# Kernel tuning notes

Hardware: AMD Instinct MI355X
Metric: run time of the kernel (lower is better)

Reference implementation:

```python
import jax, jax.numpy as jnp
import numpy as np

N = 100_000   # nodes
E = 3_200_000 # edges
F = 13        # input features
H = 64        # hidden dim
G = 512       # graphs in batch
C = 2         # output classes
BN_EPS = 1e-5


def _linear(key, fan_in, fan_out):
    kw, kb = jax.random.split(key)
    bound = 1.0 / np.sqrt(fan_in)
    W = jax.random.uniform(kw, (fan_in, fan_out), jnp.float32, -bound, bound)
    b = jax.random.uniform(kb, (fan_out,), jnp.float32, -bound, bound)
    return W, b


def _conv_params(key, fin, fout):
    k1, k2, k3 = jax.random.split(key, 3)
    W1, b1 = _linear(k1, fin, fout)
    W2, b2 = _linear(k2, fout, fout)
    gamma = jnp.ones((fout,), jnp.float32)
    beta = jnp.zeros((fout,), jnp.float32)
    mean = jax.random.normal(k3, (fout,), jnp.float32) * 0.1
    var = jnp.ones((fout,), jnp.float32)
    return W1, b1, gamma, beta, mean, var, W2, b2


def setup_inputs() -> dict:
    key = jax.random.key(0)
    ks = jax.random.split(key, 10)
    x = jax.random.normal(ks[0], (N, F), jnp.float32)
    src = jax.random.randint(ks[1], (E,), 0, N, jnp.int32)
    dst = jax.random.randint(ks[2], (E,), 0, N, jnp.int32)
    batch = jnp.sort(jax.random.randint(ks[3], (N,), 0, G, jnp.int32))
    inp = {"x": x, "src": src, "dst": dst, "batch": batch}
    for i, name in enumerate(["c1", "c2", "c3"]):
        fin = F if i == 0 else H
        W1, b1, g, be, m, v, W2, b2 = _conv_params(ks[4 + i], fin, H)
        inp.update({f"{name}_W1": W1, f"{name}_b1": b1, f"{name}_g": g,
                    f"{name}_be": be, f"{name}_m": m, f"{name}_v": v,
                    f"{name}_W2": W2, f"{name}_b2": b2})
    inp["fc1_W"], inp["fc1_b"] = _linear(ks[7], 3 * H, 3 * H)
    inp["fc2_W"], inp["fc2_b"] = _linear(ks[8], 3 * H, C)
    return inp


def _mlp(h, W1, b1, g, be, m, v, W2, b2):
    # Linear -> BatchNorm1d (inference, running stats) -> ReLU -> Linear -> ReLU
    h = h @ W1 + b1
    h = (h - m) * jax.lax.rsqrt(v + BN_EPS) * g + be
    h = jax.nn.relu(h)
    return jax.nn.relu(h @ W2 + b2)


def _gin_conv(x, src, dst, mlp_params):
    # GINConv with eps=0: MLP(x + sum_{j->i} x_j) via scatter-add over edges
    agg = jax.ops.segment_sum(x[src], dst, num_segments=N)
    return _mlp(x + agg, *mlp_params)


def reference(x, src, dst, batch,
              c1_W1, c1_b1, c1_g, c1_be, c1_m, c1_v, c1_W2, c1_b2,
              c2_W1, c2_b1, c2_g, c2_be, c2_m, c2_v, c2_W2, c2_b2,
              c3_W1, c3_b1, c3_g, c3_be, c3_m, c3_v, c3_W2, c3_b2,
              fc1_W, fc1_b, fc2_W, fc2_b):
    h1 = jax.nn.relu(_gin_conv(x, src, dst, (c1_W1, c1_b1, c1_g, c1_be, c1_m, c1_v, c1_W2, c1_b2)))
    h2 = jax.nn.relu(_gin_conv(h1, src, dst, (c2_W1, c2_b1, c2_g, c2_be, c2_m, c2_v, c2_W2, c2_b2)))
    h3 = jax.nn.relu(_gin_conv(h2, src, dst, (c3_W1, c3_b1, c3_g, c3_be, c3_m, c3_v, c3_W2, c3_b2)))
    p1 = jax.ops.segment_sum(h1, batch, num_segments=G)
    p2 = jax.ops.segment_sum(h2, batch, num_segments=G)
    p3 = jax.ops.segment_sum(h3, batch, num_segments=G)
    h = jnp.concatenate([p1, p2, p3], axis=1)  # [G, 3H]
    h = jax.nn.relu(h @ fc1_W + fc1_b)
    # Dropout is identity in eval mode
    h = h @ fc2_W + fc2_b
    return jax.nn.log_softmax(h, axis=-1)
```

## Files before the change

kernel.cpp:

```cpp
#include <hip/hip_runtime.h>

#define NNODES 100000
#define NEDGES 3200000
#define NF 13
#define NFP 16
#define NG 512
#define BN_EPS 1e-5f
#define NTILES (NNODES / 16)
#define CAP 72

#define BSH 9
#define NBUCK ((NNODES + 511) / 512)
#define RCAP 18500
#define PTILE 4096
#define NPBLK ((NEDGES + PTILE - 1) / PTILE)

#define NCHUNK ((NNODES + 63) / 64)
#define NPTASK (3 * NCHUNK)

typedef __attribute__((ext_vector_type(8))) _Float16 f16x8;
typedef __attribute__((ext_vector_type(4))) _Float16 f16x4;
typedef __attribute__((ext_vector_type(4))) float f32x4;

__device__ __forceinline__ unsigned short f2h(float f) {
    union { _Float16 h; unsigned short u; } c;
    c.h = (_Float16)f;
    return c.u;
}
__device__ __forceinline__ float h2f(unsigned short u) {
    union { _Float16 h; unsigned short u; } c;
    c.u = u;
    return (float)c.h;
}

__device__ __forceinline__ f16x8 shfl_xor8(f16x8 v, int m) {
    union { f16x8 h; int i[4]; } a, b;
    a.h = v;
#pragma unroll
    for (int k = 0; k < 4; ++k) b.i[k] = __shfl_xor(a.i[k], m, 64);
    return b.h;
}
__device__ __forceinline__ f16x4 shfl_xor4(f16x4 v, int m) {
    union { f16x4 h; int i[2]; } a, b;
    a.h = v;
#pragma unroll
    for (int k = 0; k < 2; ++k) b.i[k] = __shfl_xor(a.i[k], m, 64);
    return b.h;
}

__launch_bounds__(256)
__global__ void partition_kernel(const int* __restrict__ src, const int* __restrict__ dst,
                                 int* __restrict__ gcount, int* __restrict__ pairbuf) {
    __shared__ int lhist[NBUCK];
    __shared__ int lbase[NBUCK];
    __shared__ int lpos[NBUCK];
    int t = threadIdx.x;
    int base = blockIdx.x * PTILE;
    int cnt = NEDGES - base; if (cnt > PTILE) cnt = PTILE;

    int v[PTILE / 256], b[PTILE / 256];
#pragma unroll
    for (int j = 0; j < PTILE / 256; ++j) {
        int i = t + j * 256;
        if (i < cnt) {
            int d = __builtin_nontemporal_load(dst + base + i);
            int s = __builtin_nontemporal_load(src + base + i);
            b[j] = d >> BSH;
            v[j] = ((d & 511) << 17) | s;
        } else b[j] = -1;
    }
    if (t < NBUCK) lhist[t] = 0;
    __syncthreads();
#pragma unroll
    for (int j = 0; j < PTILE / 256; ++j)
        if (b[j] >= 0) atomicAdd(&lhist[b[j]], 1);
    __syncthreads();
    if (t < NBUCK) {
        lbase[t] = atomicAdd(&gcount[t], lhist[t]);
        lpos[t] = 0;
    }
    __syncthreads();
#pragma unroll
    for (int j = 0; j < PTILE / 256; ++j) {
        if (b[j] >= 0) {
            int p = atomicAdd(&lpos[b[j]], 1);
            pairbuf[(size_t)b[j] * RCAP + lbase[b[j]] + p] = v[j];
        }
    }
}

__launch_bounds__(512)
__global__ void bucket_scatter_kernel(const int* __restrict__ pairbuf,
                                      const int* __restrict__ gcount,
                                      int* __restrict__ cursor, int* __restrict__ csr) {
    __shared__ int lcnt[512];
    int bk = blockIdx.x;
    int lo = bk << BSH;
    int cnt = gcount[bk];
    if (threadIdx.x < 512) lcnt[threadIdx.x] = 0;
    __syncthreads();
    const int* pb = pairbuf + (size_t)bk * RCAP;
    for (int i = threadIdx.x; i < cnt; i += 512) {
        int p = pb[i];
        int s = p & 0x1FFFF;
        int dl = p >> 17;
        int pos = atomicAdd(&lcnt[dl], 1);
        csr[(size_t)(lo + dl) * CAP + pos] = s;
    }
    __syncthreads();
    int n = lo + threadIdx.x;
    if (threadIdx.x < 512 && n < NNODES) cursor[n] = n * CAP + lcnt[threadIdx.x];
}

__global__ void cvt_x_kernel(const float* __restrict__ x, unsigned short* __restrict__ xh) {
    const int total = NNODES * NFP;
    int idx = blockIdx.x * blockDim.x + threadIdx.x;
    int stride = gridDim.x * blockDim.x;
    for (int i = idx; i < total; i += stride) {
        int n = i >> 4;
        int f = i & 15;
        xh[i] = (f < NF) ? f2h(x[n * NF + f]) : (unsigned short)0;
    }
}

__global__ void build_frags_kernel(const float* __restrict__ w10, const float* __restrict__ w20,
                                   const float* __restrict__ w11, const float* __restrict__ w21,
                                   const float* __restrict__ w12, const float* __restrict__ w22,
                                   unsigned short* __restrict__ wfrag) {
    int tid = blockIdx.x * blockDim.x + threadIdx.x;
    if (tid >= 3072) return;
    int layer = tid >> 10;
    int rem = tid & 1023;
    int mat = rem >> 9;
    int tile = (rem >> 7) & 3;
    int chunk = (rem >> 6) & 1;
    int lane = rem & 63;
    int quad = lane >> 4, n = lane & 15;
    const float* W = (layer == 0) ? (mat ? w20 : w10)
                   : (layer == 1) ? (mat ? w21 : w11)
                                  : (mat ? w22 : w12);
    int K = (layer == 0 && mat == 0) ? NF : 64;
    unsigned short* o = wfrag + ((size_t)tid) * 8;
#pragma unroll
    for (int j = 0; j < 8; ++j) {
        int k = chunk * 32 + quad * 8 + j;
        float val = (k < K) ? W[k * 64 + tile * 16 + n] : 0.f;
        o[j] = f2h(val);
    }
}

template <int FSTR, int RL, int PADZ>
__launch_bounds__(256, 8)
__global__ void agg_vec_kernel(const unsigned short* __restrict__ xin,
                               const int* __restrict__ cursor,
                               const int* __restrict__ csr,
                               unsigned short* __restrict__ y) {
    const int EPG = 64 / RL;
    int lane = threadIdx.x & 63;
    int g = lane / RL;
    int r = lane % RL;
    int wave = (blockIdx.x * blockDim.x + threadIdx.x) >> 6;
    int nw = (gridDim.x * blockDim.x) >> 6;

    for (int n0 = wave * 2; n0 < NNODES; n0 += nw * 2) {
        int nA = n0, nB = n0 + 1;
        int jA = nA * CAP, endA = cursor[nA];
        int jB = nB * CAP, endB = cursor[nB];
        f16x4 accA = {0, 0, 0, 0};
        f16x4 accB = {0, 0, 0, 0};
        if (g == 0) {
            accA = *(const f16x4*)&xin[nA * FSTR + r * 4];
            accB = *(const f16x4*)&xin[nB * FSTR + r * 4];
        }
        while (jA + EPG <= endA && jB + EPG <= endB) {
            int iA = csr[jA + g];
            int iB = csr[jB + g];
            f16x4 vA = *(const f16x4*)&xin[iA * FSTR + r * 4];
            f16x4 vB = *(const f16x4*)&xin[iB * FSTR + r * 4];
            accA += vA; accB += vB;
            jA += EPG; jB += EPG;
        }
        for (; jA + 2 * EPG <= endA; jA += 2 * EPG) {
            int i0 = csr[jA + g], i1 = csr[jA + EPG + g];
            f16x4 v0 = *(const f16x4*)&xin[i0 * FSTR + r * 4];
            f16x4 v1 = *(const f16x4*)&xin[i1 * FSTR + r * 4];
            accA += v0; accA += v1;
        }
        for (; jA < endA; jA += EPG) {
            int e = jA + g;
            if (e < endA) {
                int i0 = csr[e];
                accA += *(const f16x4*)&xin[i0 * FSTR + r * 4];
            }
        }
        for (; jB + 2 * EPG <= endB; jB += 2 * EPG) {
            int i0 = csr[jB + g], i1 = csr[jB + EPG + g];
            f16x4 v0 = *(const f16x4*)&xin[i0 * FSTR + r * 4];
            f16x4 v1 = *(const f16x4*)&xin[i1 * FSTR + r * 4];
            accB += v0; accB += v1;
        }
        for (; jB < endB; jB += EPG) {
            int e = jB + g;
            if (e < endB) {
                int i0 = csr[e];
                accB += *(const f16x4*)&xin[i0 * FSTR + r * 4];
            }
        }
#pragma unroll
        for (int m = RL; m < 64; m <<= 1) {
            accA += shfl_xor4(accA, m);
            accB += shfl_xor4(accB, m);
        }
        if (g == 0) {
            *(f16x4*)&y[nA * 64 + r * 4] = accA;
            *(f16x4*)&y[nB * 64 + r * 4] = accB;
        } else if (PADZ && g == 1) {
            f16x4 z = {0, 0, 0, 0};
            *(f16x4*)&y[nA * 64 + 16 + r * 4] = z;
            *(f16x4*)&y[nB * 64 + 16 + r * 4] = z;
        }
    }
}

__launch_bounds__(256, 8)
__global__ void agg_vec8_kernel(const unsigned short* __restrict__ xin,
                                const int* __restrict__ cursor,
                                const int* __restrict__ csr,
                                unsigned short* __restrict__ y) {
    int lane = threadIdx.x & 63;
    int g = lane >> 3;
    int r = lane & 7;
    int wave = (blockIdx.x * blockDim.x + threadIdx.x) >> 6;
    int nw = (gridDim.x * blockDim.x) >> 6;

    for (int n0 = wave * 2; n0 < NNODES; n0 += nw * 2) {
        int nA = n0, nB = n0 + 1;
        int jA = nA * CAP, endA = cursor[nA];
        int jB = nB * CAP, endB = cursor[nB];
        f16x8 accA = {0, 0, 0, 0, 0, 0, 0, 0};
        f16x8 accB = {0, 0, 0, 0, 0, 0, 0, 0};
        if (g == 0) {
            accA = *(const f16x8*)&xin[(size_t)nA * 64 + r * 8];
            accB = *(const f16x8*)&xin[(size_t)nB * 64 + r * 8];
        }
        while (jA + 16 <= endA && jB + 16 <= endB) {
            int iA0 = csr[jA + g];
            int iA1 = csr[jA + 8 + g];
            int iB0 = csr[jB + g];
            int iB1 = csr[jB + 8 + g];
            f16x8 vA0 = *(const f16x8*)&xin[(size_t)iA0 * 64 + r * 8];
            f16x8 vA1 = *(const f16x8*)&xin[(size_t)iA1 * 64 + r * 8];
            f16x8 vB0 = *(const f16x8*)&xin[(size_t)iB0 * 64 + r * 8];
            f16x8 vB1 = *(const f16x8*)&xin[(size_t)iB1 * 64 + r * 8];
            accA += vA0; accA += vA1;
            accB += vB0; accB += vB1;
            jA += 16; jB += 16;
        }
        for (; jA + 16 <= endA; jA += 16) {
            int i0 = csr[jA + g], i1 = csr[jA + 8 + g];
            f16x8 v0 = *(const f16x8*)&xin[(size_t)i0 * 64 + r * 8];
            f16x8 v1 = *(const f16x8*)&xin[(size_t)i1 * 64 + r * 8];
            accA += v0; accA += v1;
        }
        for (; jA < endA; jA += 8) {
            int e = jA + g;
            if (e < endA) {
                int i0 = csr[e];
                accA += *(const f16x8*)&xin[(size_t)i0 * 64 + r * 8];
            }
        }
        for (; jB + 16 <= endB; jB += 16) {
            int i0 = csr[jB + g], i1 = csr[jB + 8 + g];
            f16x8 v0 = *(const f16x8*)&xin[(size_t)i0 * 64 + r * 8];
            f16x8 v1 = *(const f16x8*)&xin[(size_t)i1 * 64 + r * 8];
            accB += v0; accB += v1;
        }
        for (; jB < endB; jB += 8) {
            int e = jB + g;
            if (e < endB) {
                int i0 = csr[e];
                accB += *(const f16x8*)&xin[(size_t)i0 * 64 + r * 8];
            }
        }
#pragma unroll
        for (int m = 8; m < 64; m <<= 1) {
            accA += shfl_xor8(accA, m);
            accB += shfl_xor8(accB, m);
        }
        if (g == 0) {
            *(f16x8*)&y[(size_t)nA * 64 + r * 8] = accA;
            *(f16x8*)&y[(size_t)nB * 64 + r * 8] = accB;
        }
    }
}

template <int KC1>
__launch_bounds__(256)
__global__ void mlp_mfma_kernel(const unsigned short* __restrict__ yh,
                                const unsigned short* __restrict__ wfrag,
                                const float* __restrict__ b1, const float* __restrict__ g,
                                const float* __restrict__ be, const float* __restrict__ m,
                                const float* __restrict__ v,  const float* __restrict__ b2,
                                unsigned short* __restrict__ hout) {
    __shared__ __align__(16) unsigned short zs[4][16 * 72];
    int lane = threadIdx.x & 63;
    int wid = threadIdx.x >> 6;
    int quad = lane >> 4;
    int n16 = lane & 15;

    const f16x8* wf = (const f16x8*)wfrag;
    f16x8 w1f[4][2], w2f[4][2];
#pragma unroll
    for (int t = 0; t < 4; ++t) {
#pragma unroll
        for (int c = 0; c < 2; ++c) {
            w1f[t][c] = wf[((0 * 4 + t) * 2 + c) * 64 + lane];
            w2f[t][c] = wf[((1 * 4 + t) * 2 + c) * 64 + lane];
        }
    }
    float scaleF[4], shiftF[4], b2F[4];
#pragma unroll
    for (int t = 0; t < 4; ++t) {
        int f = t * 16 + n16;
        float sc = g[f] * rsqrtf(v[f] + BN_EPS);
        scaleF[t] = sc;
        shiftF[t] = (b1[f] - m[f]) * sc + be[f];
        b2F[t] = b2[f];
    }

    unsigned short* zrow = &zs[wid][0];
    int ntiles = gridDim.x * 4;
    for (int tile = blockIdx.x * 4 + wid; tile < NTILES; tile += ntiles) {
        int nodebase = tile * 16;
        const unsigned short* yrow = yh + (size_t)(nodebase + n16) * 64 + quad * 8;
        f16x8 a0 = *(const f16x8*)yrow;
        f16x8 a1 = (KC1 == 2) ? *(const f16x8*)(yrow + 32) : a0;

        f32x4 acc[4];
#pragma unroll
        for (int t = 0; t < 4; ++t) {
            f32x4 z4 = {0.f, 0.f, 0.f, 0.f};
            z4 = __builtin_amdgcn_mfma_f32_16x16x32_f16(a0, w1f[t][0], z4, 0, 0, 0);
            if (KC1 == 2)
                z4 = __builtin_amdgcn_mfma_f32_16x16x32_f16(a1, w1f[t][1], z4, 0, 0, 0);
            acc[t] = z4;
        }
#pragma unroll
        for (int t = 0; t < 4; ++t) {
#pragma unroll
            for (int r = 0; r < 4; ++r) {
                float z = fmaxf(fmaf(acc[t][r], scaleF[t], shiftF[t]), 0.f);
                zrow[(quad * 4 + r) * 72 + t * 16 + n16] = f2h(z);
            }
        }
        __threadfence_block();
        f16x8 az0 = *(const f16x8*)&zrow[n16 * 72 + quad * 8];
        f16x8 az1 = *(const f16x8*)&zrow[n16 * 72 + 32 + quad * 8];

        f32x4 acc2[4];
#pragma unroll
        for (int t = 0; t < 4; ++t) {
            f32x4 z4 = {0.f, 0.f, 0.f, 0.f};
            z4 = __builtin_amdgcn_mfma_f32_16x16x32_f16(az0, w2f[t][0], z4, 0, 0, 0);
            z4 = __builtin_amdgcn_mfma_f32_16x16x32_f16(az1, w2f[t][1], z4, 0, 0, 0);
            acc2[t] = z4;
        }
#pragma unroll
        for (int t = 0; t < 4; ++t) {
#pragma unroll
            for (int r = 0; r < 4; ++r) {
                float h = fmaxf(acc2[t][r] + b2F[t], 0.f);
                hout[(size_t)(nodebase + quad * 4 + r) * 64 + t * 16 + n16] = f2h(h);
            }
        }
        __threadfence_block();
    }
}

__launch_bounds__(256)
__global__ void pool_kernel(const unsigned short* __restrict__ h1,
                            const unsigned short* __restrict__ h2,
                            const unsigned short* __restrict__ h3,
                            const int* __restrict__ batch,
                            float* __restrict__ pool) {
    int task = blockIdx.x * 4 + (threadIdx.x >> 6);
    if (task >= NPTASK) return;
    int lane = threadIdx.x & 63;
    int layer = task / NCHUNK;
    int c = task - layer * NCHUNK;
    int n0 = c * 64;
    int n1 = n0 + 64; if (n1 > NNODES) n1 = NNODES;
    const unsigned short* hb = (layer == 0) ? h1 : (layer == 1) ? h2 : h3;
    float acc = 0.f;
    int curg = batch[n0];
    for (int n = n0; n < n1; ++n) {
        int gid = batch[n];
        if (gid != curg) {
            atomicAdd(&pool[(size_t)curg * 192 + layer * 64 + lane], acc);
            acc = 0.f;
            curg = gid;
        }
        acc += h2f(hb[(size_t)n * 64 + lane]);
    }
    atomicAdd(&pool[(size_t)curg * 192 + layer * 64 + lane], acc);
}

__global__ void head_kernel(const float* __restrict__ pool,
                            const float* __restrict__ fc1W, const float* __restrict__ fc1b,
                            const float* __restrict__ fc2W, const float* __restrict__ fc2b,
                            float* __restrict__ out) {
    __shared__ float ps[192];
    __shared__ float hs[192];
    int gi = blockIdx.x;
    int t = threadIdx.x;
    ps[t] = pool[gi * 192 + t];
    __syncthreads();
    float acc = fc1b[t];
#pragma unroll 8
    for (int k = 0; k < 192; ++k) acc = fmaf(ps[k], fc1W[k * 192 + t], acc);
    hs[t] = fmaxf(acc, 0.f);
    __syncthreads();
    if (t == 0) {
        float l0 = fc2b[0], l1 = fc2b[1];
        for (int k = 0; k < 192; ++k) {
            float h = hs[k];
            l0 = fmaf(h, fc2W[k * 2 + 0], l0);
            l1 = fmaf(h, fc2W[k * 2 + 1], l1);
        }
        float mx = fmaxf(l0, l1);
        float lse = mx + logf(expf(l0 - mx) + expf(l1 - mx));
        out[gi * 2 + 0] = l0 - lse;
        out[gi * 2 + 1] = l1 - lse;
    }
}

extern "C" void kernel_launch(void* const* d_in, const int* in_sizes, int n_in,
                              void* d_out, int out_size, void* d_ws, size_t ws_size,
                              hipStream_t stream) {
    const float* x = (const float*)d_in[0];
    const int* src = (const int*)d_in[1];
    const int* dst = (const int*)d_in[2];
    const int* batch = (const int*)d_in[3];
    const float* c1[8];
    const float* c2[8];
    const float* c3[8];
    for (int i = 0; i < 8; ++i) {
        c1[i] = (const float*)d_in[4 + i];
        c2[i] = (const float*)d_in[12 + i];
        c3[i] = (const float*)d_in[20 + i];
    }
    const float* fc1W = (const float*)d_in[28];
    const float* fc1b = (const float*)d_in[29];
    const float* fc2W = (const float*)d_in[30];
    const float* fc2b = (const float*)d_in[31];
    float* out = (float*)d_out;

    unsigned short* base = (unsigned short*)d_ws;
    const size_t NA = (size_t)NNODES * 64;
    unsigned short* yh  = base;
    unsigned short* xh  = yh + NA;
    unsigned short* h1  = xh + (size_t)NNODES * NFP;
    unsigned short* h2  = h1 + NA;
    unsigned short* h3  = h2 + NA;
    unsigned short* wfrag = h3 + NA;
    float* pool = (float*)(wfrag + 3 * 8192);
    int* ibase = (int*)(pool + (size_t)NG * 192);
    int* cursor  = ibase;
    int* gcount  = ibase + NNODES;
    int* csr     = gcount + NBUCK;
    int* pairbuf = csr + (size_t)NNODES * CAP + 256;

    hipMemsetAsync(gcount, 0, NBUCK * sizeof(int), stream);
    hipMemsetAsync(pool, 0, (size_t)NG * 192 * sizeof(float), stream);

    cvt_x_kernel<<<2048, 256, 0, stream>>>(x, xh);
    build_frags_kernel<<<12, 256, 0, stream>>>(c1[0], c1[6], c2[0], c2[6], c3[0], c3[6], wfrag);
    partition_kernel<<<NPBLK, 256, 0, stream>>>(src, dst, gcount, pairbuf);
    bucket_scatter_kernel<<<NBUCK, 512, 0, stream>>>(pairbuf, gcount, cursor, csr);

    const int AGG_BLOCKS = 12500;
    const int MLP_BLOCKS = 1024;

    agg_vec_kernel<NFP, 4, 1><<<AGG_BLOCKS, 256, 0, stream>>>(xh, cursor, csr, yh);
    mlp_mfma_kernel<1><<<MLP_BLOCKS, 256, 0, stream>>>(
        yh, wfrag + 0 * 8192, c1[1], c1[2], c1[3], c1[4], c1[5], c1[7], h1);

    agg_vec8_kernel<<<AGG_BLOCKS, 256, 0, stream>>>(h1, cursor, csr, yh);
    mlp_mfma_kernel<2><<<MLP_BLOCKS, 256, 0, stream>>>(
        yh, wfrag + 1 * 8192, c2[1], c2[2], c2[3], c2[4], c2[5], c2[7], h2);

    agg_vec8_kernel<<<AGG_BLOCKS, 256, 0, stream>>>(h2, cursor, csr, yh);
    mlp_mfma_kernel<2><<<MLP_BLOCKS, 256, 0, stream>>>(
        yh, wfrag + 2 * 8192, c3[1], c3[2], c3[3], c3[4], c3[5], c3[7], h3);

    pool_kernel<<<(NPTASK + 3) / 4, 256, 0, stream>>>(h1, h2, h3, batch, pool);
    head_kernel<<<NG, 192, 0, stream>>>(pool, fc1W, fc1b, fc2W, fc2b, out);
}
```

Baseline: 405.3 us.

## Fuse aggregation with MFMA MLP per 16-node tile and merge prep kernels

Each GIN layer now runs as one kernel: a block gathers neighbor sums for 16 nodes into shared memory, then applies both MLP matmuls with MFMA, removing the yh intermediate round trip through global memory and three launches. The preprocessing kernels (edge partition, weight fragment build, x conversion) are merged into one launch via block-index dispatch. Several read-once streams switch to nontemporal loads. The trade-off is that weights and BN constants are reloaded per 16-node block instead of amortized across a persistent grid, and occupancy is capped at 6 blocks per CU by the launch bounds.

```diff
diff --git a/kernel.cpp b/kernel.cpp
--- a/kernel.cpp
+++ b/kernel.cpp
@@ -14,6 +14,7 @@
 #define RCAP 18500
 #define PTILE 4096
 #define NPBLK ((NEDGES + PTILE - 1) / PTILE)
+#define CVTB 200
 
 #define NCHUNK ((NNODES + 63) / 64)
 #define NPTASK (3 * NCHUNK)
@@ -49,42 +50,81 @@
 }
 
 __launch_bounds__(256)
-__global__ void partition_kernel(const int* __restrict__ src, const int* __restrict__ dst,
-                                 int* __restrict__ gcount, int* __restrict__ pairbuf) {
+__global__ void prep_kernel(const int* __restrict__ src, const int* __restrict__ dst,
+                            int* __restrict__ gcount, int* __restrict__ pairbuf,
+                            const float* __restrict__ x, unsigned short* __restrict__ xh,
+                            const float* __restrict__ w10, const float* __restrict__ w20,
+                            const float* __restrict__ w11, const float* __restrict__ w21,
+                            const float* __restrict__ w12, const float* __restrict__ w22,
+                            unsigned short* __restrict__ wfrag) {
     __shared__ int lhist[NBUCK];
     __shared__ int lbase[NBUCK];
     __shared__ int lpos[NBUCK];
+    int bid = blockIdx.x;
     int t = threadIdx.x;
-    int base = blockIdx.x * PTILE;
-    int cnt = NEDGES - base; if (cnt > PTILE) cnt = PTILE;
-
-    int v[PTILE / 256], b[PTILE / 256];
-#pragma unroll
-    for (int j = 0; j < PTILE / 256; ++j) {
-        int i = t + j * 256;
-        if (i < cnt) {
-            int d = __builtin_nontemporal_load(dst + base + i);
-            int s = __builtin_nontemporal_load(src + base + i);
-            b[j] = d >> BSH;
-            v[j] = ((d & 511) << 17) | s;
-        } else b[j] = -1;
-    }
-    if (t < NBUCK) lhist[t] = 0;
-    __syncthreads();
-#pragma unroll
-    for (int j = 0; j < PTILE / 256; ++j)
-        if (b[j] >= 0) atomicAdd(&lhist[b[j]], 1);
-    __syncthreads();
-    if (t < NBUCK) {
-        lbase[t] = atomicAdd(&gcount[t], lhist[t]);
-        lpos[t] = 0;
-    }
-    __syncthreads();
-#pragma unroll
-    for (int j = 0; j < PTILE / 256; ++j) {
-        if (b[j] >= 0) {
-            int p = atomicAdd(&lpos[b[j]], 1);
-            pairbuf[(size_t)b[j] * RCAP + lbase[b[j]] + p] = v[j];
+
+    if (bid < NPBLK) {
+        int base = bid * PTILE;
+        int cnt = NEDGES - base; if (cnt > PTILE) cnt = PTILE;
+        int v[PTILE / 256], b[PTILE / 256];
+#pragma unroll
+        for (int j = 0; j < PTILE / 256; ++j) {
+            int i = t + j * 256;
+            if (i < cnt) {
+                int d = __builtin_nontemporal_load(dst + base + i);
+                int s = __builtin_nontemporal_load(src + base + i);
+                b[j] = d >> BSH;
+                v[j] = ((d & 511) << 17) | s;
+            } else b[j] = -1;
+        }
+        if (t < NBUCK) lhist[t] = 0;
+        __syncthreads();
+#pragma unroll
+        for (int j = 0; j < PTILE / 256; ++j)
+            if (b[j] >= 0) atomicAdd(&lhist[b[j]], 1);
+        __syncthreads();
+        if (t < NBUCK) {
+            lbase[t] = atomicAdd(&gcount[t], lhist[t]);
+            lpos[t] = 0;
+        }
+        __syncthreads();
+#pragma unroll
+        for (int j = 0; j < PTILE / 256; ++j) {
+            if (b[j] >= 0) {
+                int p = atomicAdd(&lpos[b[j]], 1);
+                pairbuf[(size_t)b[j] * RCAP + lbase[b[j]] + p] = v[j];
+            }
+        }
+    } else if (bid < NPBLK + 12) {
+        int tid = (bid - NPBLK) * 256 + t;
+        if (tid >= 3072) return;
+        int layer = tid >> 10;
+        int rem = tid & 1023;
+        int mat = rem >> 9;
+        int tile = (rem >> 7) & 3;
+        int chunk = (rem >> 6) & 1;
+        int lane = rem & 63;
+        int quad = lane >> 4, n = lane & 15;
+        const float* W = (layer == 0) ? (mat ? w20 : w10)
+                       : (layer == 1) ? (mat ? w21 : w11)
+                                      : (mat ? w22 : w12);
+        int K = (layer == 0 && mat == 0) ? NF : 64;
+        unsigned short* o = wfrag + ((size_t)tid) * 8;
+#pragma unroll
+        for (int j = 0; j < 8; ++j) {
+            int k = chunk * 32 + quad * 8 + j;
+            float val = (k < K) ? W[k * 64 + tile * 16 + n] : 0.f;
+            o[j] = f2h(val);
+        }
+    } else {
+        const int total = NNODES * NFP;
+        int idx = (bid - NPBLK - 12) * 256 + t;
+        int stride = CVTB * 256;
+        for (int i = idx; i < total; i += stride) {
+            int n = i >> 4;
+            int f = i & 15;
+            xh[i] = (f < NF) ? f2h(__builtin_nontemporal_load(x + n * NF + f))
+                             : (unsigned short)0;
         }
     }
 }
@@ -101,7 +141,7 @@
     __syncthreads();
     const int* pb = pairbuf + (size_t)bk * RCAP;
     for (int i = threadIdx.x; i < cnt; i += 512) {
-        int p = pb[i];
+        int p = __builtin_nontemporal_load(pb + i);
         int s = p & 0x1FFFF;
         int dl = p >> 17;
         int pos = atomicAdd(&lcnt[dl], 1);
@@ -112,268 +152,194 @@
     if (threadIdx.x < 512 && n < NNODES) cursor[n] = n * CAP + lcnt[threadIdx.x];
 }
 
-__global__ void cvt_x_kernel(const float* __restrict__ x, unsigned short* __restrict__ xh) {
-    const int total = NNODES * NFP;
-    int idx = blockIdx.x * blockDim.x + threadIdx.x;
-    int stride = gridDim.x * blockDim.x;
-    for (int i = idx; i < total; i += stride) {
-        int n = i >> 4;
-        int f = i & 15;
-        xh[i] = (f < NF) ? f2h(x[n * NF + f]) : (unsigned short)0;
-    }
-}
-
-__global__ void build_frags_kernel(const float* __restrict__ w10, const float* __restrict__ w20,
-                                   const float* __restrict__ w11, const float* __restrict__ w21,
-                                   const float* __restrict__ w12, const float* __restrict__ w22,
-                                   unsigned short* __restrict__ wfrag) {
-    int tid = blockIdx.x * blockDim.x + threadIdx.x;
-    if (tid >= 3072) return;
-    int layer = tid >> 10;
-    int rem = tid & 1023;
-    int mat = rem >> 9;
-    int tile = (rem >> 7) & 3;
-    int chunk = (rem >> 6) & 1;
-    int lane = rem & 63;
-    int quad = lane >> 4, n = lane & 15;
-    const float* W = (layer == 0) ? (mat ? w20 : w10)
-                   : (layer == 1) ? (mat ? w21 : w11)
-                                  : (mat ? w22 : w12);
-    int K = (layer == 0 && mat == 0) ? NF : 64;
-    unsigned short* o = wfrag + ((size_t)tid) * 8;
-#pragma unroll
-    for (int j = 0; j < 8; ++j) {
-        int k = chunk * 32 + quad * 8 + j;
-        float val = (k < K) ? W[k * 64 + tile * 16 + n] : 0.f;
-        o[j] = f2h(val);
-    }
-}
-
-template <int FSTR, int RL, int PADZ>
-__launch_bounds__(256, 8)
-__global__ void agg_vec_kernel(const unsigned short* __restrict__ xin,
-                               const int* __restrict__ cursor,
-                               const int* __restrict__ csr,
-                               unsigned short* __restrict__ y) {
-    const int EPG = 64 / RL;
-    int lane = threadIdx.x & 63;
-    int g = lane / RL;
-    int r = lane % RL;
-    int wave = (blockIdx.x * blockDim.x + threadIdx.x) >> 6;
-    int nw = (gridDim.x * blockDim.x) >> 6;
-
-    for (int n0 = wave * 2; n0 < NNODES; n0 += nw * 2) {
-        int nA = n0, nB = n0 + 1;
-        int jA = nA * CAP, endA = cursor[nA];
-        int jB = nB * CAP, endB = cursor[nB];
-        f16x4 accA = {0, 0, 0, 0};
-        f16x4 accB = {0, 0, 0, 0};
-        if (g == 0) {
-            accA = *(const f16x4*)&xin[nA * FSTR + r * 4];
-            accB = *(const f16x4*)&xin[nB * FSTR + r * 4];
-        }
-        while (jA + EPG <= endA && jB + EPG <= endB) {
-            int iA = csr[jA + g];
-            int iB = csr[jB + g];
-            f16x4 vA = *(const f16x4*)&xin[iA * FSTR + r * 4];
-            f16x4 vB = *(const f16x4*)&xin[iB * FSTR + r * 4];
-            accA += vA; accB += vB;
-            jA += EPG; jB += EPG;
-        }
-        for (; jA + 2 * EPG <= endA; jA += 2 * EPG) {
-            int i0 = csr[jA + g], i1 = csr[jA + EPG + g];
-            f16x4 v0 = *(const f16x4*)&xin[i0 * FSTR + r * 4];
-            f16x4 v1 = *(const f16x4*)&xin[i1 * FSTR + r * 4];
-            accA += v0; accA += v1;
-        }
-        for (; jA < endA; jA += EPG) {
-            int e = jA + g;
-            if (e < endA) {
-                int i0 = csr[e];
-                accA += *(const f16x4*)&xin[i0 * FSTR + r * 4];
-            }
-        }
-        for (; jB + 2 * EPG <= endB; jB += 2 * EPG) {
-            int i0 = csr[jB + g], i1 = csr[jB + EPG + g];
-            f16x4 v0 = *(const f16x4*)&xin[i0 * FSTR + r * 4];
-            f16x4 v1 = *(const f16x4*)&xin[i1 * FSTR + r * 4];
-            accB += v0; accB += v1;
-        }
-        for (; jB < endB; jB += EPG) {
-            int e = jB + g;
-            if (e < endB) {
-                int i0 = csr[e];
-                accB += *(const f16x4*)&xin[i0 * FSTR + r * 4];
-            }
-        }
-#pragma unroll
-        for (int m = RL; m < 64; m <<= 1) {
-            accA += shfl_xor4(accA, m);
-            accB += shfl_xor4(accB, m);
-        }
-        if (g == 0) {
-            *(f16x4*)&y[nA * 64 + r * 4] = accA;
-            *(f16x4*)&y[nB * 64 + r * 4] = accB;
-        } else if (PADZ && g == 1) {
-            f16x4 z = {0, 0, 0, 0};
-            *(f16x4*)&y[nA * 64 + 16 + r * 4] = z;
-            *(f16x4*)&y[nB * 64 + 16 + r * 4] = z;
-        }
-    }
-}
-
-__launch_bounds__(256, 8)
-__global__ void agg_vec8_kernel(const unsigned short* __restrict__ xin,
-                                const int* __restrict__ cursor,
-                                const int* __restrict__ csr,
-                                unsigned short* __restrict__ y) {
-    int lane = threadIdx.x & 63;
-    int g = lane >> 3;
-    int r = lane & 7;
-    int wave = (blockIdx.x * blockDim.x + threadIdx.x) >> 6;
-    int nw = (gridDim.x * blockDim.x) >> 6;
-
-    for (int n0 = wave * 2; n0 < NNODES; n0 += nw * 2) {
-        int nA = n0, nB = n0 + 1;
-        int jA = nA * CAP, endA = cursor[nA];
-        int jB = nB * CAP, endB = cursor[nB];
-        f16x8 accA = {0, 0, 0, 0, 0, 0, 0, 0};
-        f16x8 accB = {0, 0, 0, 0, 0, 0, 0, 0};
-        if (g == 0) {
-            accA = *(const f16x8*)&xin[(size_t)nA * 64 + r * 8];
-            accB = *(const f16x8*)&xin[(size_t)nB * 64 + r * 8];
-        }
-        while (jA + 16 <= endA && jB + 16 <= endB) {
-            int iA0 = csr[jA + g];
-            int iA1 = csr[jA + 8 + g];
-            int iB0 = csr[jB + g];
-            int iB1 = csr[jB + 8 + g];
-            f16x8 vA0 = *(const f16x8*)&xin[(size_t)iA0 * 64 + r * 8];
-            f16x8 vA1 = *(const f16x8*)&xin[(size_t)iA1 * 64 + r * 8];
-            f16x8 vB0 = *(const f16x8*)&xin[(size_t)iB0 * 64 + r * 8];
-            f16x8 vB1 = *(const f16x8*)&xin[(size_t)iB1 * 64 + r * 8];
-            accA += vA0; accA += vA1;
-            accB += vB0; accB += vB1;
-            jA += 16; jB += 16;
-        }
-        for (; jA + 16 <= endA; jA += 16) {
-            int i0 = csr[jA + g], i1 = csr[jA + 8 + g];
-            f16x8 v0 = *(const f16x8*)&xin[(size_t)i0 * 64 + r * 8];
-            f16x8 v1 = *(const f16x8*)&xin[(size_t)i1 * 64 + r * 8];
-            accA += v0; accA += v1;
-        }
-        for (; jA < endA; jA += 8) {
-            int e = jA + g;
-            if (e < endA) {
-                int i0 = csr[e];
-                accA += *(const f16x8*)&xin[(size_t)i0 * 64 + r * 8];
-            }
-        }
-        for (; jB + 16 <= endB; jB += 16) {
-            int i0 = csr[jB + g], i1 = csr[jB + 8 + g];
-            f16x8 v0 = *(const f16x8*)&xin[(size_t)i0 * 64 + r * 8];
-            f16x8 v1 = *(const f16x8*)&xin[(size_t)i1 * 64 + r * 8];
-            accB += v0; accB += v1;
-        }
-        for (; jB < endB; jB += 8) {
-            int e = jB + g;
-            if (e < endB) {
-                int i0 = csr[e];
-                accB += *(const f16x8*)&xin[(size_t)i0 * 64 + r * 8];
-            }
-        }
-#pragma unroll
-        for (int m = 8; m < 64; m <<= 1) {
-            accA += shfl_xor8(accA, m);
-            accB += shfl_xor8(accB, m);
-        }
-        if (g == 0) {
-            *(f16x8*)&y[(size_t)nA * 64 + r * 8] = accA;
-            *(f16x8*)&y[(size_t)nB * 64 + r * 8] = accB;
-        }
-    }
-}
-
-template <int KC1>
-__launch_bounds__(256)
-__global__ void mlp_mfma_kernel(const unsigned short* __restrict__ yh,
-                                const unsigned short* __restrict__ wfrag,
-                                const float* __restrict__ b1, const float* __restrict__ g,
-                                const float* __restrict__ be, const float* __restrict__ m,
-                                const float* __restrict__ v,  const float* __restrict__ b2,
-                                unsigned short* __restrict__ hout) {
-    __shared__ __align__(16) unsigned short zs[4][16 * 72];
+template <int LAYER>
+__launch_bounds__(256, 6)
+__global__ void gin_layer_kernel(const unsigned short* __restrict__ xin,
+                                 const int* __restrict__ cursor,
+                                 const int* __restrict__ csr,
+                                 const unsigned short* __restrict__ wfrag,
+                                 const float* __restrict__ b1, const float* __restrict__ gam,
+                                 const float* __restrict__ be, const float* __restrict__ mu,
+                                 const float* __restrict__ var, const float* __restrict__ b2,
+                                 unsigned short* __restrict__ hout) {
+    constexpr int FSTR = (LAYER == 1) ? NFP : 64;
+    __shared__ __align__(16) unsigned short ytile[16][80];
+    __shared__ __align__(16) unsigned short ztile[16][80];
     int lane = threadIdx.x & 63;
     int wid = threadIdx.x >> 6;
-    int quad = lane >> 4;
-    int n16 = lane & 15;
+    int quad = lane >> 4, n16 = lane & 15;
+    int nb = blockIdx.x * 16;
+
+    if constexpr (LAYER == 1) {
+        int g = lane >> 2;
+        int r = lane & 3;
+#pragma unroll
+        for (int pp = 0; pp < 2; ++pp) {
+            int lnA = wid * 4 + pp * 2;
+            int nA = nb + lnA, nB = nA + 1;
+            int jA = nA * CAP, jB = nB * CAP;
+            int endA = __builtin_nontemporal_load(cursor + nA);
+            int endB = __builtin_nontemporal_load(cursor + nB);
+            f16x4 accA = {0, 0, 0, 0};
+            f16x4 accB = {0, 0, 0, 0};
+            if (g == 0) {
+                accA = *(const f16x4*)&xin[(size_t)nA * FSTR + r * 4];
+                accB = *(const f16x4*)&xin[(size_t)nB * FSTR + r * 4];
+            }
+            while (jA + 16 <= endA && jB + 16 <= endB) {
+                int iA = __builtin_nontemporal_load(csr + jA + g);
+                int iB = __builtin_nontemporal_load(csr + jB + g);
+                f16x4 vA = *(const f16x4*)&xin[(size_t)iA * FSTR + r * 4];
+                f16x4 vB = *(const f16x4*)&xin[(size_t)iB * FSTR + r * 4];
+                accA += vA; accB += vB;
+                jA += 16; jB += 16;
+            }
+            for (; jA + 32 <= endA; jA += 32) {
+                int i0 = __builtin_nontemporal_load(csr + jA + g);
+                int i1 = __builtin_nontemporal_load(csr + jA + 16 + g);
+                f16x4 v0 = *(const f16x4*)&xin[(size_t)i0 * FSTR + r * 4];
+                f16x4 v1 = *(const f16x4*)&xin[(size_t)i1 * FSTR + r * 4];
+                accA += v0; accA += v1;
+            }
+            for (; jA < endA; jA += 16) {
+                int e = jA + g;
+                if (e < endA) {
+                    int i0 = __builtin_nontemporal_load(csr + e);
+                    accA += *(const f16x4*)&xin[(size_t)i0 * FSTR + r * 4];
+                }
+            }
+            for (; jB + 32 <= endB; jB += 32) {
+                int i0 = __builtin_nontemporal_load(csr + jB + g);
+                int i1 = __builtin_nontemporal_load(csr + jB + 16 + g);
+                f16x4 v0 = *(const f16x4*)&xin[(size_t)i0 * FSTR + r * 4];
+                f16x4 v1 = *(const f16x4*)&xin[(size_t)i1 * FSTR + r * 4];
+                accB += v0; accB += v1;
+            }
+            for (; jB < endB; jB += 16) {
+                int e = jB + g;
+                if (e < endB) {
+                    int i0 = __builtin_nontemporal_load(csr + e);
+                    accB += *(const f16x4*)&xin[(size_t)i0 * FSTR + r * 4];
+                }
+            }
+#pragma unroll
+            for (int m = 4; m < 64; m <<= 1) {
+                accA += shfl_xor4(accA, m);
+                accB += shfl_xor4(accB, m);
+            }
+            if (g == 0) {
+                *(f16x4*)&ytile[lnA][r * 4] = accA;
+                *(f16x4*)&ytile[lnA + 1][r * 4] = accB;
+            } else if (g == 1) {
+                f16x4 z = {0, 0, 0, 0};
+                *(f16x4*)&ytile[lnA][16 + r * 4] = z;
+                *(f16x4*)&ytile[lnA + 1][16 + r * 4] = z;
+            }
+        }
+    } else {
+        int g = lane >> 3;
+        int r = lane & 7;
+#pragma unroll
+        for (int pp = 0; pp < 2; ++pp) {
+            int lnA = wid * 4 + pp * 2;
+            int nA = nb + lnA, nB = nA + 1;
+            int jA = nA * CAP, jB = nB * CAP;
+            int endA = __builtin_nontemporal_load(cursor + nA);
+            int endB = __builtin_nontemporal_load(cursor + nB);
+            f16x8 accA = {0, 0, 0, 0, 0, 0, 0, 0};
+            f16x8 accB = {0, 0, 0, 0, 0, 0, 0, 0};
+            if (g == 0) {
+                accA = *(const f16x8*)&xin[(size_t)nA * 64 + r * 8];
+                accB = *(const f16x8*)&xin[(size_t)nB * 64 + r * 8];
+            }
+            while (jA + 16 <= endA && jB + 16 <= endB) {
+                int iA0 = __builtin_nontemporal_load(csr + jA + g);
+                int iA1 = __builtin_nontemporal_load(csr + jA + 8 + g);
+                int iB0 = __builtin_nontemporal_load(csr + jB + g);
+                int iB1 = __builtin_nontemporal_load(csr + jB + 8 + g);
+                f16x8 vA0 = *(const f16x8*)&xin[(size_t)iA0 * 64 + r * 8];
+                f16x8 vA1 = *(const f16x8*)&xin[(size_t)iA1 * 64 + r * 8];
+                f16x8 vB0 = *(const f16x8*)&xin[(size_t)iB0 * 64 + r * 8];
+                f16x8 vB1 = *(const f16x8*)&xin[(size_t)iB1 * 64 + r * 8];
+                accA += vA0; accA += vA1;
+                accB += vB0; accB += vB1;
+                jA += 16; jB += 16;
+            }
+            for (; jA + 16 <= endA; jA += 16) {
+                int i0 = __builtin_nontemporal_load(csr + jA + g);
+                int i1 = __builtin_nontemporal_load(csr + jA + 8 + g);
+                f16x8 v0 = *(const f16x8*)&xin[(size_t)i0 * 64 + r * 8];
+                f16x8 v1 = *(const f16x8*)&xin[(size_t)i1 * 64 + r * 8];
+                accA += v0; accA += v1;
+            }
+            for (; jA < endA; jA += 8) {
+                int e = jA + g;
+                if (e < endA) {
+                    int i0 = __builtin_nontemporal_load(csr + e);
+                    accA += *(const f16x8*)&xin[(size_t)i0 * 64 + r * 8];
+                }
+            }
+            for (; jB + 16 <= endB; jB += 16) {
+                int i0 = __builtin_nontemporal_load(csr + jB + g);
+                int i1 = __builtin_nontemporal_load(csr + jB + 8 + g);
+                f16x8 v0 = *(const f16x8*)&xin[(size_t)i0 * 64 + r * 8];
+                f16x8 v1 = *(const f16x8*)&xin[(size_t)i1 * 64 + r * 8];
+                accB += v0; accB += v1;
+            }
+            for (; jB < endB; jB += 8) {
+                int e = jB + g;
+                if (e < endB) {
+                    int i0 = __builtin_nontemporal_load(csr + e);
+                    accB += *(const f16x8*)&xin[(size_t)i0 * 64 + r * 8];
+                }
+            }
+#pragma unroll
+            for (int m = 8; m < 64; m <<= 1) {
+                accA += shfl_xor8(accA, m);
+                accB += shfl_xor8(accB, m);
+            }
+            if (g == 0) {
+                *(f16x8*)&ytile[lnA][r * 8] = accA;
+                *(f16x8*)&ytile[lnA + 1][r * 8] = accB;
+            }
+        }
+    }
 
     const f16x8* wf = (const f16x8*)wfrag;
-    f16x8 w1f[4][2], w2f[4][2];
-#pragma unroll
-    for (int t = 0; t < 4; ++t) {
-#pragma unroll
-        for (int c = 0; c < 2; ++c) {
-            w1f[t][c] = wf[((0 * 4 + t) * 2 + c) * 64 + lane];
-            w2f[t][c] = wf[((1 * 4 + t) * 2 + c) * 64 + lane];
-        }
-    }
-    float scaleF[4], shiftF[4], b2F[4];
-#pragma unroll
-    for (int t = 0; t < 4; ++t) {
-        int f = t * 16 + n16;
-        float sc = g[f] * rsqrtf(v[f] + BN_EPS);
-        scaleF[t] = sc;
-        shiftF[t] = (b1[f] - m[f]) * sc + be[f];
-        b2F[t] = b2[f];
-    }
-
-    unsigned short* zrow = &zs[wid][0];
-    int ntiles = gridDim.x * 4;
-    for (int tile = blockIdx.x * 4 + wid; tile < NTILES; tile += ntiles) {
-        int nodebase = tile * 16;
-        const unsigned short* yrow = yh + (size_t)(nodebase + n16) * 64 + quad * 8;
-        f16x8 a0 = *(const f16x8*)yrow;
-        f16x8 a1 = (KC1 == 2) ? *(const f16x8*)(yrow + 32) : a0;
-
-        f32x4 acc[4];
-#pragma unroll
-        for (int t = 0; t < 4; ++t) {
-            f32x4 z4 = {0.f, 0.f, 0.f, 0.f};
-            z4 = __builtin_amdgcn_mfma_f32_16x16x32_f16(a0, w1f[t][0], z4, 0, 0, 0);
-            if (KC1 == 2)
-                z4 = __builtin_amdgcn_mfma_f32_16x16x32_f16(a1, w1f[t][1], z4, 0, 0, 0);
-            acc[t] = z4;
-        }
-#pragma unroll
-        for (int t = 0; t < 4; ++t) {
-#pragma unroll
-            for (int r = 0; r < 4; ++r) {
-                float z = fmaxf(fmaf(acc[t][r], scaleF[t], shiftF[t]), 0.f);
-                zrow[(quad * 4 + r) * 72 + t * 16 + n16] = f2h(z);
-            }
-        }
-        __threadfence_block();
-        f16x8 az0 = *(const f16x8*)&zrow[n16 * 72 + quad * 8];
-        f16x8 az1 = *(const f16x8*)&zrow[n16 * 72 + 32 + quad * 8];
-
-        f32x4 acc2[4];
-#pragma unroll
-        for (int t = 0; t < 4; ++t) {
-            f32x4 z4 = {0.f, 0.f, 0.f, 0.f};
-            z4 = __builtin_amdgcn_mfma_f32_16x16x32_f16(az0, w2f[t][0], z4, 0, 0, 0);
-            z4 = __builtin_amdgcn_mfma_f32_16x16x32_f16(az1, w2f[t][1], z4, 0, 0, 0);
-            acc2[t] = z4;
-        }
-#pragma unroll
-        for (int t = 0; t < 4; ++t) {
-#pragma unroll
-            for (int r = 0; r < 4; ++r) {
-                float h = fmaxf(acc2[t][r] + b2F[t], 0.f);
-                hout[(size_t)(nodebase + quad * 4 + r) * 64 + t * 16 + n16] = f2h(h);
-            }
-        }
-        __threadfence_block();
+    f16x8 w1f0 = wf[((0 * 4 + wid) * 2 + 0) * 64 + lane];
+    f16x8 w1f1 = (LAYER == 2) ? wf[((0 * 4 + wid) * 2 + 1) * 64 + lane] : w1f0;
+    f16x8 w2f0 = wf[((1 * 4 + wid) * 2 + 0) * 64 + lane];
+    f16x8 w2f1 = wf[((1 * 4 + wid) * 2 + 1) * 64 + lane];
+    int f = wid * 16 + n16;
+    float sc = gam[f] * rsqrtf(var[f] + BN_EPS);
+    float sh = (b1[f] - mu[f]) * sc + be[f];
+    float bb2 = b2[f];
+
+    __syncthreads();
+
+    f16x8 a0 = *(const f16x8*)&ytile[n16][quad * 8];
+    f32x4 z4 = {0.f, 0.f, 0.f, 0.f};
+    z4 = __builtin_amdgcn_mfma_f32_16x16x32_f16(a0, w1f0, z4, 0, 0, 0);
+    if constexpr (LAYER == 2) {
+        f16x8 a1 = *(const f16x8*)&ytile[n16][32 + quad * 8];
+        z4 = __builtin_amdgcn_mfma_f32_16x16x32_f16(a1, w1f1, z4, 0, 0, 0);
+    }
+#pragma unroll
+    for (int reg = 0; reg < 4; ++reg) {
+        float z = fmaxf(fmaf(z4[reg], sc, sh), 0.f);
+        ztile[quad * 4 + reg][wid * 16 + n16] = f2h(z);
+    }
+    __syncthreads();
+
+    f16x8 az0 = *(const f16x8*)&ztile[n16][quad * 8];
+    f16x8 az1 = *(const f16x8*)&ztile[n16][32 + quad * 8];
+    f32x4 h4 = {0.f, 0.f, 0.f, 0.f};
+    h4 = __builtin_amdgcn_mfma_f32_16x16x32_f16(az0, w2f0, h4, 0, 0, 0);
+    h4 = __builtin_amdgcn_mfma_f32_16x16x32_f16(az1, w2f1, h4, 0, 0, 0);
+#pragma unroll
+    for (int reg = 0; reg < 4; ++reg) {
+        float h = fmaxf(h4[reg] + bb2, 0.f);
+        hout[(size_t)(nb + quad * 4 + reg) * 64 + wid * 16 + n16] = f2h(h);
     }
 }
 
@@ -400,7 +366,7 @@
             acc = 0.f;
             curg = gid;
         }
-        acc += h2f(hb[(size_t)n * 64 + lane]);
+        acc += h2f(__builtin_nontemporal_load(hb + (size_t)n * 64 + lane));
     }
     atomicAdd(&pool[(size_t)curg * 192 + layer * 64 + lane], acc);
 }
@@ -457,8 +423,7 @@
 
     unsigned short* base = (unsigned short*)d_ws;
     const size_t NA = (size_t)NNODES * 64;
-    unsigned short* yh  = base;
-    unsigned short* xh  = yh + NA;
+    unsigned short* xh  = base;
     unsigned short* h1  = xh + (size_t)NNODES * NFP;
     unsigned short* h2  = h1 + NA;
     unsigned short* h3  = h2 + NA;
@@ -473,25 +438,20 @@
     hipMemsetAsync(gcount, 0, NBUCK * sizeof(int), stream);
     hipMemsetAsync(pool, 0, (size_t)NG * 192 * sizeof(float), stream);
 
-    cvt_x_kernel<<<2048, 256, 0, stream>>>(x, xh);
-    build_frags_kernel<<<12, 256, 0, stream>>>(c1[0], c1[6], c2[0], c2[6], c3[0], c3[6], wfrag);
-    partition_kernel<<<NPBLK, 256, 0, stream>>>(src, dst, gcount, pairbuf);
+    prep_kernel<<<NPBLK + 12 + CVTB, 256, 0, stream>>>(
+        src, dst, gcount, pairbuf, x, xh,
+        c1[0], c1[6], c2[0], c2[6], c3[0], c3[6], wfrag);
     bucket_scatter_kernel<<<NBUCK, 512, 0, stream>>>(pairbuf, gcount, cursor, csr);
 
-    const int AGG_BLOCKS = 12500;
-    const int MLP_BLOCKS = 1024;
-
-    agg_vec_kernel<NFP, 4, 1><<<AGG_BLOCKS, 256, 0, stream>>>(xh, cursor, csr, yh);
-    mlp_mfma_kernel<1><<<MLP_BLOCKS, 256, 0, stream>>>(
-        yh, wfrag + 0 * 8192, c1[1], c1[2], c1[3], c1[4], c1[5], c1[7], h1);
-
-    agg_vec8_kernel<<<AGG_BLOCKS, 256, 0, stream>>>(h1, cursor, csr, yh);
-    mlp_mfma_kernel<2><<<MLP_BLOCKS, 256, 0, stream>>>(
-        yh, wfrag + 1 * 8192, c2[1], c2[2], c2[3], c2[4], c2[5], c2[7], h2);
-
-    agg_vec8_kernel<<<AGG_BLOCKS, 256, 0, stream>>>(h2, cursor, csr, yh);
-    mlp_mfma_kernel<2><<<MLP_BLOCKS, 256, 0, stream>>>(
-        yh, wfrag + 2 * 8192, c3[1], c3[2], c3[3], c3[4], c3[5], c3[7], h3);
+    gin_layer_kernel<1><<<NTILES, 256, 0, stream>>>(
+        xh, cursor, csr, wfrag + 0 * 8192,
+        c1[1], c1[2], c1[3], c1[4], c1[5], c1[7], h1);
+    gin_layer_kernel<2><<<NTILES, 256, 0, stream>>>(
+        h1, cursor, csr, wfrag + 1 * 8192,
+        c2[1], c2[2], c2[3], c2[4], c2[5], c2[7], h2);
+    gin_layer_kernel<2><<<NTILES, 256, 0, stream>>>(
+        h2, cursor, csr, wfrag + 2 * 8192,
+        c3[1], c3[2], c3[3], c3[4], c3[5], c3[7], h3);
 
     pool_kernel<<<(NPTASK + 3) / 4, 256, 0, stream>>>(h1, h2, h3, batch, pool);
     head_kernel<<<NG, 192, 0, stream>>>(pool, fc1W, fc1b, fc2W, fc2b, out);
```

Result: no change. 407.7 us (+0.6%).
